# Optimization experiments

Hardware: AMD Instinct MI355X
Metric: run time of the kernel (lower is better)

## Reference

```python
import jax, jax.numpy as jnp
import numpy as np

B, T_TXT = 16, 2048
ALPHA = 1.0


def setup_inputs() -> dict:
    key = jax.random.key(0)
    k1, _ = jax.random.split(key)
    # durations in frames per text token, 1..15 (randint per spec, cast to float)
    dur = jax.random.randint(k1, (B, T_TXT), 1, 16).astype(jnp.float32)
    dur_padding = jnp.zeros((B, T_TXT), dtype=jnp.int32)
    return {"dur": dur, "dur_padding": dur_padding}


def reference(dur, dur_padding):
    # Faithful to LengthRegulator.forward with alpha=1.0.
    # Original builds a (B, T_txt, T_speech) boolean mask and reduces it;
    # mathematically mel2ph[b, t] = 1 + #{j : dur_cumsum[b, j] <= t} for
    # t < total[b], else 0 (disjoint token intervals), which is exactly
    # searchsorted(dur_cumsum, t, side='right') + 1.
    d = jnp.round(dur * ALPHA).astype(jnp.int32)
    d = d * (1 - dur_padding)                    # zero out padded tokens
    dur_cumsum = jnp.cumsum(d, axis=1)            # (B, T_txt)
    total = dur_cumsum[:, -1]                     # (B,) total frames per item
    T_speech = int(jnp.max(total))                # data-dependent out length
    pos = jnp.arange(T_speech, dtype=jnp.int32)   # (T_speech,)
    # per-batch binary search: token index (0-based) owning each frame
    tok = jax.vmap(lambda c: jnp.searchsorted(c, pos, side="right"))(dur_cumsum)
    mel2ph = jnp.where(pos[None, :] < total[:, None], tok + 1, 0)
    return mel2ph.astype(jnp.int32)               # (B, T_speech)
```

## Files before the change

kernel.cpp:

```cpp
#include <hip/hip_runtime.h>

#define T_TXT 2048
#define TPB 1024
#define NWAVE (TPB / 64)

__global__ __launch_bounds__(TPB) void length_regulator_kernel(
    const float* __restrict__ dur,
    const int*   __restrict__ dur_padding,
    int*         __restrict__ out,
    int T_speech)
{
    __shared__ int c[T_TXT];
    __shared__ int wsum[NWAVE];

    const int row  = blockIdx.x;
    const int tid  = threadIdx.x;
    const int lane = tid & 63;
    const int wid  = tid >> 6;

    const float* drow = dur         + (size_t)row * T_TXT;
    const int*   prow = dur_padding + (size_t)row * T_TXT;

    const int i0 = tid * 2;
    float f0 = drow[i0];
    float f1 = drow[i0 + 1];
    int   p0 = prow[i0];
    int   p1 = prow[i0 + 1];
    int d0 = (int)rintf(f0) * (1 - p0);
    int d1 = (int)rintf(f1) * (1 - p1);

    int s0 = d0;
    int s1 = d0 + d1;

    int incl = s1;
    #pragma unroll
    for (int off = 1; off < 64; off <<= 1) {
        int up = __shfl_up(incl, off, 64);
        if (lane >= off) incl += up;
    }
    int excl = incl - s1;
    if (lane == 63) wsum[wid] = incl;
    __syncthreads();

    int woff = 0, total = 0;
    #pragma unroll
    for (int w = 0; w < NWAVE; ++w) {
        int v = wsum[w];
        total += v;
        if (w < wid) woff += v;
    }

    const int base = woff + excl;
    c[i0]     = base + s0;
    c[i0 + 1] = base + s1;
    __syncthreads();

    int* orow = out + (size_t)row * T_speech;
    #pragma unroll
    for (int it = 0; it < T_TXT / TPB; ++it) {
        const int t     = tid + it * TPB;
        const int start = (t == 0) ? 0 : c[t - 1];
        const int end   = c[t];
        const int val   = t + 1;
        for (int p = start; p < end; ++p) orow[p] = val;
    }

    for (int p = total + tid; p < T_speech; p += TPB) orow[p] = 0;
}

extern "C" void kernel_launch(void* const* d_in, const int* in_sizes, int n_in,
                              void* d_out, int out_size, void* d_ws, size_t ws_size,
                              hipStream_t stream) {
    (void)n_in; (void)d_ws; (void)ws_size;
    const float* dur         = (const float*)d_in[0];
    const int*   dur_padding = (const int*)d_in[1];
    int*         out         = (int*)d_out;

    const int B        = in_sizes[0] / T_TXT;
    const int T_speech = out_size / B;

    length_regulator_kernel<<<B, TPB, 0, stream>>>(dur, dur_padding, out, T_speech);
}
```

Measured before the change: 58.62 us.

## Split each row's output writes across 16 blocks with redundant per-block scan

Launches a 2D grid (B x 16 slices) of 256-thread blocks instead of one 1024-thread block per row. Each block redundantly recomputes the full row cumsum using vectorized float4/int4 loads with 8 elements per thread, then writes only its 128-token slice of the output and a strided share of the zero tail. This spreads the scattered output stores over many more CUs, at the cost of 16x redundant input reads and scans, and only 128 of 256 threads do output writes.

```diff
diff --git a/kernel.cpp b/kernel.cpp
--- a/kernel.cpp
+++ b/kernel.cpp
@@ -1,8 +1,11 @@
 #include <hip/hip_runtime.h>
 
-#define T_TXT 2048
-#define TPB 1024
-#define NWAVE (TPB / 64)
+#define T_TXT  2048
+#define TPB    256
+#define EPT    (T_TXT / TPB)
+#define NWAVE  (TPB / 64)
+#define NSLICE 16
+#define TOK_PER_SLICE (T_TXT / NSLICE)
 
 __global__ __launch_bounds__(TPB) void length_regulator_kernel(
     const float* __restrict__ dur,
@@ -13,32 +16,38 @@
     __shared__ int c[T_TXT];
     __shared__ int wsum[NWAVE];
 
-    const int row  = blockIdx.x;
-    const int tid  = threadIdx.x;
-    const int lane = tid & 63;
-    const int wid  = tid >> 6;
+    const int row   = blockIdx.x;
+    const int slice = blockIdx.y;
+    const int tid   = threadIdx.x;
+    const int lane  = tid & 63;
+    const int wid   = tid >> 6;
 
     const float* drow = dur         + (size_t)row * T_TXT;
     const int*   prow = dur_padding + (size_t)row * T_TXT;
 
-    const int i0 = tid * 2;
-    float f0 = drow[i0];
-    float f1 = drow[i0 + 1];
-    int   p0 = prow[i0];
-    int   p1 = prow[i0 + 1];
-    int d0 = (int)rintf(f0) * (1 - p0);
-    int d1 = (int)rintf(f1) * (1 - p1);
+    const int i0 = tid * EPT;
+    const float4 f0 = ((const float4*)(drow + i0))[0];
+    const float4 f1 = ((const float4*)(drow + i0))[1];
+    const int4   p0 = ((const int4*)(prow + i0))[0];
+    const int4   p1 = ((const int4*)(prow + i0))[1];
 
-    int s0 = d0;
-    int s1 = d0 + d1;
+    int s[EPT];
+    s[0] = (int)rintf(f0.x) * (1 - p0.x);
+    s[1] = s[0] + (int)rintf(f0.y) * (1 - p0.y);
+    s[2] = s[1] + (int)rintf(f0.z) * (1 - p0.z);
+    s[3] = s[2] + (int)rintf(f0.w) * (1 - p0.w);
+    s[4] = s[3] + (int)rintf(f1.x) * (1 - p1.x);
+    s[5] = s[4] + (int)rintf(f1.y) * (1 - p1.y);
+    s[6] = s[5] + (int)rintf(f1.z) * (1 - p1.z);
+    s[7] = s[6] + (int)rintf(f1.w) * (1 - p1.w);
 
-    int incl = s1;
+    int incl = s[EPT - 1];
     #pragma unroll
     for (int off = 1; off < 64; off <<= 1) {
         int up = __shfl_up(incl, off, 64);
         if (lane >= off) incl += up;
     }
-    int excl = incl - s1;
+    const int excl = incl - s[EPT - 1];
     if (lane == 63) wsum[wid] = incl;
     __syncthreads();
 
@@ -51,21 +60,21 @@
     }
 
     const int base = woff + excl;
-    c[i0]     = base + s0;
-    c[i0 + 1] = base + s1;
+    #pragma unroll
+    for (int j = 0; j < EPT; ++j) c[i0 + j] = base + s[j];
     __syncthreads();
 
     int* orow = out + (size_t)row * T_speech;
-    #pragma unroll
-    for (int it = 0; it < T_TXT / TPB; ++it) {
-        const int t     = tid + it * TPB;
+    if (tid < TOK_PER_SLICE) {
+        const int t     = slice * TOK_PER_SLICE + tid;
         const int start = (t == 0) ? 0 : c[t - 1];
         const int end   = c[t];
         const int val   = t + 1;
         for (int p = start; p < end; ++p) orow[p] = val;
     }
 
-    for (int p = total + tid; p < T_speech; p += TPB) orow[p] = 0;
+    for (int p = total + slice * TPB + tid; p < T_speech; p += NSLICE * TPB)
+        orow[p] = 0;
 }
 
 extern "C" void kernel_launch(void* const* d_in, const int* in_sizes, int n_in,
@@ -79,5 +88,6 @@
     const int B        = in_sizes[0] / T_TXT;
     const int T_speech = out_size / B;
 
-    length_regulator_kernel<<<B, TPB, 0, stream>>>(dur, dur_padding, out, T_speech);
+    dim3 grid(B, NSLICE);
+    length_regulator_kernel<<<grid, TPB, 0, stream>>>(dur, dur_padding, out, T_speech);
 }
```

New measurement: 56.12 us. -4.3%, faster.
